# Performance work log

Measured on AMD Instinct MI355X. Metric: run time of the kernel, lower is better.

Reference implementation:

```python
import jax, jax.numpy as jnp
import numpy as np

N_NODES = 10000
N_EDGES = 160000
F_IN = 2613
D = 256
H = 4
NEG_SLOPE = 0.2
BN_EPS = 1e-5


def _bn(h, g, b):
    # BatchNorm1d in training mode: batch statistics, biased variance
    return (h - h.mean(0)) / jnp.sqrt(h.var(0) + BN_EPS) * g + b


def _gat_conv(h_in, src, dst, n, W, att_src, att_dst, bias):
    # PyG GATConv, concat=True: h_in [n, F] -> [n, H*D]
    h = (h_in @ W).reshape(n, H, D)                      # [n, H, D]
    a_src = jnp.sum(h * att_src, axis=-1)                # [n, H]
    a_dst = jnp.sum(h * att_dst, axis=-1)                # [n, H]
    e = jax.nn.leaky_relu(a_src[src] + a_dst[dst], NEG_SLOPE)  # [E, H]
    # segment softmax over destination nodes (stable)
    m = jax.ops.segment_max(e, dst, num_segments=n)
    e = jnp.exp(e - m[dst])
    denom = jax.ops.segment_sum(e, dst, num_segments=n)
    alpha = e / (denom[dst] + 1e-16)                     # [E, H]
    out = jax.ops.segment_sum(h[src] * alpha[:, :, None], dst, num_segments=n)
    return out.reshape(n, H * D) + bias


def setup_inputs() -> dict:
    key = jax.random.key(0)
    ks = jax.random.split(key, 24)
    s = 0.02
    inp = {
        "x": jax.random.normal(ks[0], (N_NODES, F_IN), jnp.float32),
        "edges": jax.random.randint(ks[1], (2, N_EDGES), 0, N_NODES, jnp.int64),
        # MLP stack
        "W1": jax.random.normal(ks[2], (F_IN, D), jnp.float32) * s,
        "b1": jnp.zeros((D,), jnp.float32),
        "W2": jax.random.normal(ks[3], (D, D), jnp.float32) * s,
        "b2": jnp.zeros((D,), jnp.float32),
        "W3": jax.random.normal(ks[4], (D, D), jnp.float32) * s,
        "b3": jnp.zeros((D,), jnp.float32),
        # BatchNorm affine params
        "g1": jnp.ones((D,), jnp.float32), "be1": jnp.zeros((D,), jnp.float32),
        "g2": jnp.ones((D,), jnp.float32), "be2": jnp.zeros((D,), jnp.float32),
        "g3": jnp.ones((D,), jnp.float32), "be3": jnp.zeros((D,), jnp.float32),
        "g4": jnp.ones((H * D,), jnp.float32), "be4": jnp.zeros((H * D,), jnp.float32),
        "Wg1": jax.random.normal(ks[5], (D, H * D), jnp.float32) * s,
        "as1": jax.random.normal(ks[6], (H, D), jnp.float32) * s,
        "ad1": jax.random.normal(ks[7], (H, D), jnp.float32) * s,
        "bg1": jnp.zeros((H * D,), jnp.float32),
        "Wg2": jax.random.normal(ks[8], (H * D, H * D), jnp.float32) * s,
        "as2": jax.random.normal(ks[9], (H, D), jnp.float32) * s,
        "ad2": jax.random.normal(ks[10], (H, D), jnp.float32) * s,
        "bg2": jnp.zeros((H * D,), jnp.float32),
    }
    return inp


def reference(x, edges, W1, b1, W2, b2, W3, b3,
              g1, be1, g2, be2, g3, be3, g4, be4,
              Wg1, as1, ad1, bg1, Wg2, as2, ad2, bg2):
    n = x.shape[0]
    src, dst = edges[0], edges[1]
    # PyG: remove existing self-loops then add one per node. We reroute
    # accidental self-loops deterministically, then append self-loops.
    dst = jnp.where(src == dst, (dst + 1) % n, dst)
    loops = jnp.arange(n, dtype=src.dtype)
    src = jnp.concatenate([src, loops])
    dst = jnp.concatenate([dst, loops])

    h = jax.nn.elu(_bn(x @ W1 + b1, g1, be1))
    h = jax.nn.elu(_bn(h @ W2 + b2, g2, be2))
    h = jax.nn.elu(_bn(h @ W3 + b3, g3, be3))
    h = _gat_conv(h, src, dst, n, Wg1, as1, ad1, bg1)
    h = jax.nn.elu(_bn(h, g4, be4))
    h = _gat_conv(h, src, dst, n, Wg2, as2, ad2, bg2)
    return h
```

## Files before the change

kernel.cpp:

```cpp
#include <hip/hip_runtime.h>
#include <hip/hip_bf16.h>

typedef __attribute__((ext_vector_type(8))) short short8v;
typedef __attribute__((ext_vector_type(4))) float f32x4;

__device__ inline float b2f(ushort u) {
  union { uint i; float f; } c;
  c.i = (uint)u << 16;
  return c.f;
}
__device__ inline ushort f2b(float f) {
  __hip_bfloat16 h = __float2bfloat16(f);
  return *(ushort*)&h;
}

typedef __attribute__((address_space(1))) const unsigned int guint;
typedef __attribute__((address_space(3))) unsigned int luint;
__device__ __forceinline__ void gload16(const void* g, void* l) {
  __builtin_amdgcn_global_load_lds((guint*)g, (luint*)l, 16, 0, 0);
}

template <bool BN, bool ALIGNED, bool SPLIT>
__global__ __launch_bounds__(256) void gemm_bn(
    const float* __restrict__ A, const __hip_bfloat16* __restrict__ Bh,
    const __hip_bfloat16* __restrict__ Bl, const float* __restrict__ sc,
    const float* __restrict__ sh, float* __restrict__ P, int M, int N, int K,
    int Kp, int nc, int nr, int nz) {
  __shared__ ushort Ash[128][40];
  __shared__ ushort Asl[SPLIT ? 128 : 1][40];
  __shared__ ushort Bs2[2][128][32];
  __shared__ ushort Bl2[SPLIT ? 2 : 1][128][32];
  const int nwg = gridDim.x;
  const int b = blockIdx.x;
  const int l = (b & 7) * (nwg >> 3) + (b >> 3);
  const int cb = l % nc;
  const int rr = (l / nc) % nr;
  const int z = l / (nc * nr);

  const int tid = threadIdx.x;
  const int lane = tid & 63;
  const int w = tid >> 6, wr = w >> 1, wc = w & 1;
  const int brow = rr * 128, bcol = cb * 128;
  const int l15 = lane & 15, koff = (lane >> 4) * 8;
  const int arow = tid >> 1, aseg = (tid & 1) * 16;
  const int srow = tid >> 2, sseg = (tid & 3) * 8;
  const int nK = (K + 31) >> 5;
  const int ks0 = (nK * z) / nz, ks1 = (nK * (z + 1)) / nz;

  f32x4 acc[4][4] = {};

  const int ar = brow + arow;
  const bool arv = ar < M;
  const float* Arow = A + (long)ar * K;
  const ushort* gBh0 = (const ushort*)Bh + (long)(bcol + srow) * Kp + sseg;
  const ushort* gBh1 = (const ushort*)Bh + (long)(bcol + 64 + srow) * Kp + sseg;
  const ushort* gBl0 = SPLIT ? (const ushort*)Bl + (long)(bcol + srow) * Kp + sseg : nullptr;
  const ushort* gBl1 = SPLIT ? (const ushort*)Bl + (long)(bcol + 64 + srow) * Kp + sseg : nullptr;
  const int lo0 = (w * 64) << 3;
  const int lo1 = (256 + w * 64) << 3;

  float av[16];
  auto loadAv = [&](int ks) {
    const int kb = (ks << 5) + aseg;
    if (arv) {
      if (ALIGNED) {
        const float4* ap = (const float4*)(Arow + kb);
#pragma unroll
        for (int q = 0; q < 4; ++q) {
          float4 f = ap[q];
          av[q * 4 + 0] = f.x;
          av[q * 4 + 1] = f.y;
          av[q * 4 + 2] = f.z;
          av[q * 4 + 3] = f.w;
        }
      } else {
        if (kb + 16 <= K) {
#pragma unroll
          for (int j = 0; j < 16; ++j) av[j] = Arow[kb + j];
        } else {
#pragma unroll
          for (int j = 0; j < 16; ++j) av[j] = (kb + j < K) ? Arow[kb + j] : 0.f;
        }
      }
    } else {
#pragma unroll
      for (int j = 0; j < 16; ++j) av[j] = 0.f;
    }
  };

  if (ks0 < ks1) {
    loadAv(ks0);
    const int k0 = ks0 << 5;
    gload16(gBh0 + k0, &Bs2[0][0][0] + lo0);
    gload16(gBh1 + k0, &Bs2[0][0][0] + lo1);
    if (SPLIT) {
      gload16(gBl0 + k0, &Bl2[0][0][0] + lo0);
      gload16(gBl1 + k0, &Bl2[0][0][0] + lo1);
    }
  }

  for (int ks = ks0; ks < ks1; ++ks) {
    const int cur = (ks - ks0) & 1;
    const int kbase = (ks << 5) + aseg;
    if (BN && arv) {
#pragma unroll
      for (int q = 0; q < 4; ++q) {
        float4 c4 = *(const float4*)(sc + kbase + q * 4);
        float4 h4 = *(const float4*)(sh + kbase + q * 4);
        float* a4 = &av[q * 4];
        a4[0] = fmaf(a4[0], c4.x, h4.x);
        a4[1] = fmaf(a4[1], c4.y, h4.y);
        a4[2] = fmaf(a4[2], c4.z, h4.z);
        a4[3] = fmaf(a4[3], c4.w, h4.w);
      }
#pragma unroll
      for (int j = 0; j < 16; ++j) {
        float v = av[j];
        av[j] = v > 0.f ? v : (__expf(v) - 1.f);
      }
    }
    short8v ah0, ah1, al0, al1;
    if (SPLIT) {
#pragma unroll
      for (int j = 0; j < 8; ++j) {
        {
          uint u = __float_as_uint(av[j]);
          ah0[j] = (short)(u >> 16);
          al0[j] = (short)f2b(av[j] - __uint_as_float(u & 0xFFFF0000u));
        }
        {
          uint u = __float_as_uint(av[j + 8]);
          ah1[j] = (short)(u >> 16);
          al1[j] = (short)f2b(av[j + 8] - __uint_as_float(u & 0xFFFF0000u));
        }
      }
    } else {
#pragma unroll
      for (int j = 0; j < 8; ++j) {
        ah0[j] = (short)f2b(av[j]);
        ah1[j] = (short)f2b(av[j + 8]);
      }
    }
    __syncthreads();
    *(short8v*)&Ash[arow][aseg] = ah0;
    *(short8v*)&Ash[arow][aseg + 8] = ah1;
    if (SPLIT) {
      *(short8v*)&Asl[arow][aseg] = al0;
      *(short8v*)&Asl[arow][aseg + 8] = al1;
    }
    __syncthreads();
    if (ks + 1 < ks1) {
      const int k0n = (ks + 1) << 5;
      const int nxt = cur ^ 1;
      gload16(gBh0 + k0n, &Bs2[nxt][0][0] + lo0);
      gload16(gBh1 + k0n, &Bs2[nxt][0][0] + lo1);
      if (SPLIT) {
        gload16(gBl0 + k0n, &Bl2[nxt][0][0] + lo0);
        gload16(gBl1 + k0n, &Bl2[nxt][0][0] + lo1);
      }
      loadAv(ks + 1);
    }
    short8v bfh[4], bfl[4];
#pragma unroll
    for (int nn = 0; nn < 4; ++nn) {
      bfh[nn] = *(const short8v*)&Bs2[cur][wc * 64 + nn * 16 + l15][koff];
      if (SPLIT) bfl[nn] = *(const short8v*)&Bl2[cur][wc * 64 + nn * 16 + l15][koff];
    }
#pragma unroll
    for (int m = 0; m < 4; ++m) {
      short8v afh = *(const short8v*)&Ash[wr * 64 + m * 16 + l15][koff];
      short8v afl;
      if (SPLIT) afl = *(const short8v*)&Asl[wr * 64 + m * 16 + l15][koff];
#pragma unroll
      for (int nn = 0; nn < 4; ++nn) {
        acc[m][nn] = __builtin_amdgcn_mfma_f32_16x16x32_bf16(afh, bfh[nn], acc[m][nn], 0, 0, 0);
        if (SPLIT) {
          acc[m][nn] = __builtin_amdgcn_mfma_f32_16x16x32_bf16(afh, bfl[nn], acc[m][nn], 0, 0, 0);
          acc[m][nn] = __builtin_amdgcn_mfma_f32_16x16x32_bf16(afl, bfh[nn], acc[m][nn], 0, 0, 0);
        }
      }
    }
  }

  float* outp = P + (long)z * M * N;
#pragma unroll
  for (int m = 0; m < 4; ++m) {
#pragma unroll
    for (int nn = 0; nn < 4; ++nn) {
      int col = bcol + wc * 64 + nn * 16 + l15;
#pragma unroll
      for (int r = 0; r < 4; ++r) {
        int row = brow + wr * 64 + m * 16 + (lane >> 4) * 4 + r;
        if (row < M) outp[(long)row * N + col] = acc[m][nn][r];
      }
    }
  }
}

__global__ __launch_bounds__(256) void gemm_bf16(
    const ushort* __restrict__ A, const __hip_bfloat16* __restrict__ B,
    ushort* __restrict__ C, int M, int N, int K, int nc, int nr) {
  __shared__ ushort A2[2][128][32];
  __shared__ ushort B2[2][128][32];
  const int nwg = gridDim.x;
  const int b = blockIdx.x;
  const int l = (b & 7) * (nwg >> 3) + (b >> 3);
  const int cb = l % nc;
  const int rr = l / nc;

  const int tid = threadIdx.x;
  const int lane = tid & 63;
  const int w = tid >> 6, wr = w >> 1, wc = w & 1;
  const int brow = rr * 128, bcol = cb * 128;
  const int l15 = lane & 15, koff = (lane >> 4) * 8;
  const int srow = tid >> 2, sseg = (tid & 3) * 8;
  const int nK = K >> 5;

  f32x4 acc[4][4] = {};

  const ushort* gA0 = A + (long)(brow + srow) * K + sseg;
  const ushort* gA1 = A + (long)(brow + 64 + srow) * K + sseg;
  const ushort* gB0 = (const ushort*)B + (long)(bcol + srow) * K + sseg;
  const ushort* gB1 = (const ushort*)B + (long)(bcol + 64 + srow) * K + sseg;
  const int lo0 = (w * 64) << 3;
  const int lo1 = (256 + w * 64) << 3;

  gload16(gA0, &A2[0][0][0] + lo0);
  gload16(gA1, &A2[0][0][0] + lo1);
  gload16(gB0, &B2[0][0][0] + lo0);
  gload16(gB1, &B2[0][0][0] + lo1);

  for (int ks = 0; ks < nK; ++ks) {
    const int cur = ks & 1;
    __syncthreads();
    if (ks + 1 < nK) {
      const int k0n = (ks + 1) << 5;
      const int nxt = cur ^ 1;
      gload16(gA0 + k0n, &A2[nxt][0][0] + lo0);
      gload16(gA1 + k0n, &A2[nxt][0][0] + lo1);
      gload16(gB0 + k0n, &B2[nxt][0][0] + lo0);
      gload16(gB1 + k0n, &B2[nxt][0][0] + lo1);
    }
    short8v bf[4];
#pragma unroll
    for (int nn = 0; nn < 4; ++nn)
      bf[nn] = *(const short8v*)&B2[cur][wc * 64 + nn * 16 + l15][koff];
#pragma unroll
    for (int m = 0; m < 4; ++m) {
      short8v af = *(const short8v*)&A2[cur][wr * 64 + m * 16 + l15][koff];
#pragma unroll
      for (int nn = 0; nn < 4; ++nn)
        acc[m][nn] = __builtin_amdgcn_mfma_f32_16x16x32_bf16(af, bf[nn], acc[m][nn], 0, 0, 0);
    }
  }

#pragma unroll
  for (int m = 0; m < 4; ++m) {
#pragma unroll
    for (int nn = 0; nn < 4; ++nn) {
      int col = bcol + wc * 64 + nn * 16 + l15;
#pragma unroll
      for (int r = 0; r < 4; ++r) {
        int row = brow + wr * 64 + m * 16 + (lane >> 4) * 4 + r;
        if (row < M) C[(long)row * N + col] = f2b(acc[m][nn][r]);
      }
    }
  }
}

__global__ __launch_bounds__(256) void bn_elu_b16(
    const float* __restrict__ h, const float* __restrict__ sc,
    const float* __restrict__ sh, ushort* __restrict__ o, long MN, int N) {
  long nq = MN >> 2;
  for (long q = blockIdx.x * 256LL + threadIdx.x; q < nq;
       q += (long)gridDim.x * 256LL) {
    long i = q << 2;
    int col = (int)(i % N);
    float4 v = *(const float4*)(h + i);
    float4 c = *(const float4*)(sc + col);
    float4 s = *(const float4*)(sh + col);
    float a0 = fmaf(v.x, c.x, s.x);
    float a1 = fmaf(v.y, c.y, s.y);
    float a2 = fmaf(v.z, c.z, s.z);
    float a3 = fmaf(v.w, c.w, s.w);
    a0 = a0 > 0.f ? a0 : (__expf(a0) - 1.f);
    a1 = a1 > 0.f ? a1 : (__expf(a1) - 1.f);
    a2 = a2 > 0.f ? a2 : (__expf(a2) - 1.f);
    a3 = a3 > 0.f ? a3 : (__expf(a3) - 1.f);
    ushort4 r;
    r.x = f2b(a0);
    r.y = f2b(a1);
    r.z = f2b(a2);
    r.w = f2b(a3);
    *(ushort4*)(o + i) = r;
  }
}

template <bool BIAS, bool STATS>
__global__ __launch_bounds__(256) void reduce_post(
    const float* __restrict__ P, const float* __restrict__ bias,
    float* __restrict__ C, float* __restrict__ osum, float* __restrict__ osq,
    long MN, int N, int Z) {
  const int col = (int)((blockIdx.x * 256 + threadIdx.x) % N);
  const float bv = BIAS ? bias[col] : 0.f;
  float ps = 0.f, pq = 0.f;
  for (long i = blockIdx.x * 256LL + threadIdx.x; i < MN;
       i += (long)gridDim.x * 256LL) {
    float s = bv;
    for (int zz = 0; zz < Z; ++zz) s += P[(long)zz * MN + i];
    C[i] = s;
    if (STATS) {
      ps += s;
      pq += s * s;
    }
  }
  if (STATS) {
    atomicAdd(&osum[col], ps);
    atomicAdd(&osq[col], pq);
  }
}

__global__ __launch_bounds__(256) void bn_coef(
    const float* __restrict__ ssum, const float* __restrict__ ssq,
    const float* __restrict__ g, const float* __restrict__ be,
    float* __restrict__ sc, float* __restrict__ sh, int N, float invM) {
  int c = blockIdx.x * 256 + threadIdx.x;
  if (c >= N) return;
  float mean = ssum[c] * invM;
  float var = ssq[c] * invM - mean * mean;
  float s = rsqrtf(var + 1e-5f) * g[c];
  sc[c] = s;
  sh[c] = be[c] - mean * s;
}

template <bool LO>
__global__ __launch_bounds__(256) void trans_split(
    const float* __restrict__ W, __hip_bfloat16* __restrict__ Oh,
    __hip_bfloat16* __restrict__ Ol, int K, int N, int Kp) {
  __shared__ float tile[64][65];
  const int k0 = blockIdx.x * 64, n0 = blockIdx.y * 64;
  const int tx = threadIdx.x & 63, ty = threadIdx.x >> 6;
#pragma unroll
  for (int j = 0; j < 16; ++j) {
    int r = ty * 16 + j;
    int k = k0 + r;
    tile[r][tx] = (k < K) ? W[(long)k * N + n0 + tx] : 0.f;
  }
  __syncthreads();
#pragma unroll
  for (int j = 0; j < 16; ++j) {
    int a = ty * 16 + j;
    float v = tile[tx][a];
    long o = (long)(n0 + a) * Kp + k0 + tx;
    if (LO) {
      uint u = __float_as_uint(v);
      ushort hu = (ushort)(u >> 16);
      Oh[o] = *(__hip_bfloat16*)&hu;
      ushort lu = f2b(v - __uint_as_float(u & 0xFFFF0000u));
      Ol[o] = *(__hip_bfloat16*)&lu;
    } else {
      ushort hu = f2b(v);
      Oh[o] = *(__hip_bfloat16*)&hu;
    }
  }
}

__global__ __launch_bounds__(256) void bn_stats(
    const float* __restrict__ h, int M, int N, float* __restrict__ sum,
    float* __restrict__ sumsq) {
  int col = blockIdx.y * 256 + threadIdx.x;
  float s = 0.f, sq = 0.f;
  for (int r = blockIdx.x; r < M; r += gridDim.x) {
    float v = h[(long)r * N + col];
    s += v;
    sq += v * v;
  }
  atomicAdd(&sum[col], s);
  atomicAdd(&sumsq[col], sq);
}

__global__ __launch_bounds__(256) void att_scores_bf16(
    const ushort* __restrict__ hgb, const float* __restrict__ att_s,
    const float* __restrict__ att_d, float* __restrict__ a_src,
    float* __restrict__ a_dst, int n) {
  int node = blockIdx.x;
  int h = threadIdx.x >> 6, lane = threadIdx.x & 63;
  int c = lane * 4;
  ushort4 hv = *(const ushort4*)(hgb + (long)node * 1024 + h * 256 + c);
  float4 as = *(const float4*)(att_s + h * 256 + c);
  float4 ad = *(const float4*)(att_d + h * 256 + c);
  float x0 = b2f(hv.x), x1 = b2f(hv.y), x2 = b2f(hv.z), x3 = b2f(hv.w);
  float ss = x0 * as.x + x1 * as.y + x2 * as.z + x3 * as.w;
  float sd = x0 * ad.x + x1 * ad.y + x2 * ad.z + x3 * ad.w;
#pragma unroll
  for (int off = 32; off; off >>= 1) {
    ss += __shfl_down(ss, off);
    sd += __shfl_down(sd, off);
  }
  if (lane == 0) {
    a_src[node * 4 + h] = ss;
    a_dst[node * 4 + h] = sd;
  }
}

__global__ __launch_bounds__(256) void deg_count(
    const int* __restrict__ srcA, const int* __restrict__ dstA,
    int* __restrict__ deg, int n, int E0, int E) {
  int e = blockIdx.x * blockDim.x + threadIdx.x;
  if (e >= E) return;
  int d;
  if (e < E0) {
    int s = srcA[e];
    d = dstA[e];
    if (s == d) d = (d + 1) % n;
  } else {
    d = e - E0;
  }
  atomicAdd(&deg[d], 1);
}

__global__ __launch_bounds__(256) void scan_rows(
    const int* __restrict__ deg, int* __restrict__ row_start, int n) {
  __shared__ int sums[256];
  int t = threadIdx.x;
  int chunk = (n + 255) / 256;
  int start = t * chunk, end = min(start + chunk, n);
  int s = 0;
  for (int i = start; i < end; ++i) s += deg[i];
  sums[t] = s;
  __syncthreads();
  for (int off = 1; off < 256; off <<= 1) {
    int v = (t >= off) ? sums[t - off] : 0;
    __syncthreads();
    sums[t] += v;
    __syncthreads();
  }
  int run = (t == 0) ? 0 : sums[t - 1];
  for (int i = start; i < end; ++i) {
    row_start[i] = run;
    run += deg[i];
  }
  if (t == 255) row_start[n] = run;
}

__global__ __launch_bounds__(256) void scatter_edges(
    const int* __restrict__ srcA, const int* __restrict__ dstA,
    int* __restrict__ cursor, int* __restrict__ csr_src, int n, int E0, int E) {
  int e = blockIdx.x * blockDim.x + threadIdx.x;
  if (e >= E) return;
  int s, d;
  if (e < E0) {
    s = srcA[e];
    d = dstA[e];
    if (s == d) d = (d + 1) % n;
  } else {
    s = d = e - E0;
  }
  int pos = atomicAdd(&cursor[d], 1);
  csr_src[pos] = s;
}

__global__ __launch_bounds__(256) void aggregate_fused(
    const ushort* __restrict__ hgb, const int* __restrict__ row_start,
    const int* __restrict__ csr_src, const float* __restrict__ a_src,
    const float* __restrict__ a_dst, const float* __restrict__ bias,
    float* __restrict__ out) {
  int d = blockIdx.x;
  int t = threadIdx.x;
  int hh = t >> 6;
  int off = hh * 256 + (t & 63) * 4;
  int p0 = row_start[d], p1 = row_start[d + 1];
  float adv = a_dst[d * 4 + hh];
  float den = 1e-16f;
  float4 acc = {0.f, 0.f, 0.f, 0.f};
  for (int p = p0; p < p1; ++p) {
    int s = csr_src[p];
    float v = a_src[s * 4 + hh] + adv;
    v = v > 0.f ? v : 0.2f * v;
    float ex = __expf(v);
    den += ex;
    ushort4 hv = *(const ushort4*)(hgb + (long)s * 1024 + off);
    acc.x += ex * b2f(hv.x);
    acc.y += ex * b2f(hv.y);
    acc.z += ex * b2f(hv.z);
    acc.w += ex * b2f(hv.w);
  }
  float rden = 1.f / den;
  float4 bv = *(const float4*)(bias + off);
  float4 o;
  o.x = bv.x + acc.x * rden;
  o.y = bv.y + acc.y * rden;
  o.z = bv.z + acc.z * rden;
  o.w = bv.w + acc.w * rden;
  *(float4*)(out + (long)d * 1024 + off) = o;
}

extern "C" void kernel_launch(void* const* d_in, const int* in_sizes, int n_in,
                              void* d_out, int out_size, void* d_ws,
                              size_t ws_size, hipStream_t stream) {
  const float* x = (const float*)d_in[0];
  const int* edges = (const int*)d_in[1];
  const float* W1 = (const float*)d_in[2];
  const float* b1 = (const float*)d_in[3];
  const float* W2 = (const float*)d_in[4];
  const float* b2 = (const float*)d_in[5];
  const float* W3 = (const float*)d_in[6];
  const float* b3 = (const float*)d_in[7];
  const float* g1 = (const float*)d_in[8];
  const float* be1 = (const float*)d_in[9];
  const float* g2 = (const float*)d_in[10];
  const float* be2 = (const float*)d_in[11];
  const float* g3 = (const float*)d_in[12];
  const float* be3 = (const float*)d_in[13];
  const float* g4 = (const float*)d_in[14];
  const float* be4 = (const float*)d_in[15];
  const float* Wg1 = (const float*)d_in[16];
  const float* as1 = (const float*)d_in[17];
  const float* ad1 = (const float*)d_in[18];
  const float* bg1 = (const float*)d_in[19];
  const float* Wg2 = (const float*)d_in[20];
  const float* as2 = (const float*)d_in[21];
  const float* ad2 = (const float*)d_in[22];
  const float* bg2 = (const float*)d_in[23];
  float* out = (float*)d_out;

  const int n = 10000, E0 = 160000, E = 170000;
  const int F = 2613, Fp = 2624, D = 256, HD = 1024;
  const int* srcA = edges;
  const int* dstA = edges + E0;

  uint8_t* p = (uint8_t*)d_ws;
  auto alloc = [&](size_t bytes) -> void* {
    void* r = (void*)p;
    p += (bytes + 255) & ~(size_t)255;
    return r;
  };
  float* h1 = (float*)alloc((size_t)n * D * 4);
  float* h2 = (float*)alloc((size_t)n * D * 4);
  float* h3 = (float*)alloc((size_t)n * D * 4);
  float* agg = (float*)alloc((size_t)n * HD * 4);
  float* pbuf = (float*)alloc((size_t)4 * n * D * 4);
  ushort* hgb = (ushort*)alloc((size_t)n * HD * 2);
  ushort* actb = (ushort*)alloc((size_t)n * HD * 2);
  __hip_bfloat16* W1h = (__hip_bfloat16*)alloc((size_t)D * Fp * 2);
  __hip_bfloat16* W2h = (__hip_bfloat16*)alloc((size_t)D * D * 2);
  __hip_bfloat16* W2l = (__hip_bfloat16*)alloc((size_t)D * D * 2);
  __hip_bfloat16* W3h = (__hip_bfloat16*)alloc((size_t)D * D * 2);
  __hip_bfloat16* W3l = (__hip_bfloat16*)alloc((size_t)D * D * 2);
  __hip_bfloat16* Wg1h = (__hip_bfloat16*)alloc((size_t)HD * D * 2);
  __hip_bfloat16* Wg2h = (__hip_bfloat16*)alloc((size_t)HD * HD * 2);
  float* asrc = (float*)alloc((size_t)n * 4 * 4);
  float* adst = (float*)alloc((size_t)n * 4 * 4);
  float* sc1 = (float*)alloc(D * 4);
  float* sh1 = (float*)alloc(D * 4);
  float* sc2 = (float*)alloc(D * 4);
  float* sh2 = (float*)alloc(D * 4);
  float* sc3 = (float*)alloc(D * 4);
  float* sh3 = (float*)alloc(D * 4);
  float* sc4 = (float*)alloc(HD * 4);
  float* sh4 = (float*)alloc(HD * 4);
  int* row_start = (int*)alloc((size_t)(n + 1) * 4);
  int* cursor = (int*)alloc((size_t)n * 4);
  int* csr_src = (int*)alloc((size_t)E * 4);
  uint8_t* z0 = p;
  float* ssum1 = (float*)alloc(D * 4);
  float* ssq1 = (float*)alloc(D * 4);
  float* ssum2 = (float*)alloc(D * 4);
  float* ssq2 = (float*)alloc(D * 4);
  float* ssum3 = (float*)alloc(D * 4);
  float* ssq3 = (float*)alloc(D * 4);
  float* ssum4 = (float*)alloc(HD * 4);
  float* ssq4 = (float*)alloc(HD * 4);
  int* deg = (int*)alloc((size_t)n * 4);
  size_t zbytes = (size_t)(p - z0);

  dim3 blk(256);
  const int rb = (n + 127) / 128;
  const int eb = (E + 255) / 256;
  const long MN_D = (long)n * D;
  const long MN_HD = (long)n * HD;
  const float invM = 1.f / (float)n;
  const int gMLP = 2 * rb * 4;
  const int gGAT = 8 * rb;

  hipMemsetAsync(z0, 0, zbytes, stream);

  deg_count<<<eb, blk, 0, stream>>>(srcA, dstA, deg, n, E0, E);
  scan_rows<<<1, blk, 0, stream>>>(deg, row_start, n);
  hipMemcpyAsync(cursor, row_start, n * sizeof(int), hipMemcpyDeviceToDevice, stream);
  scatter_edges<<<eb, blk, 0, stream>>>(srcA, dstA, cursor, csr_src, n, E0, E);

  trans_split<false><<<dim3(Fp / 64, D / 64), blk, 0, stream>>>(W1, W1h, nullptr, F, D, Fp);
  trans_split<true><<<dim3(D / 64, D / 64), blk, 0, stream>>>(W2, W2h, W2l, D, D, D);
  trans_split<true><<<dim3(D / 64, D / 64), blk, 0, stream>>>(W3, W3h, W3l, D, D, D);
  trans_split<false><<<dim3(D / 64, HD / 64), blk, 0, stream>>>(Wg1, Wg1h, nullptr, D, HD, D);
  trans_split<false><<<dim3(HD / 64, HD / 64), blk, 0, stream>>>(Wg2, Wg2h, nullptr, HD, HD, HD);

  gemm_bn<false, false, false><<<gMLP, blk, 0, stream>>>(
      x, W1h, nullptr, nullptr, nullptr, pbuf, n, D, F, Fp, 2, rb, 4);
  reduce_post<true, true><<<512, blk, 0, stream>>>(pbuf, b1, h1, ssum1, ssq1, MN_D, D, 4);
  bn_coef<<<1, blk, 0, stream>>>(ssum1, ssq1, g1, be1, sc1, sh1, D, invM);

  gemm_bn<true, true, true><<<gMLP, blk, 0, stream>>>(
      h1, W2h, W2l, sc1, sh1, pbuf, n, D, D, D, 2, rb, 4);
  reduce_post<true, true><<<512, blk, 0, stream>>>(pbuf, b2, h2, ssum2, ssq2, MN_D, D, 4);
  bn_coef<<<1, blk, 0, stream>>>(ssum2, ssq2, g2, be2, sc2, sh2, D, invM);

  gemm_bn<true, true, true><<<gMLP, blk, 0, stream>>>(
      h2, W3h, W3l, sc2, sh2, pbuf, n, D, D, D, 2, rb, 4);
  reduce_post<true, true><<<512, blk, 0, stream>>>(pbuf, b3, h3, ssum3, ssq3, MN_D, D, 4);
  bn_coef<<<1, blk, 0, stream>>>(ssum3, ssq3, g3, be3, sc3, sh3, D, invM);

  bn_elu_b16<<<1024, blk, 0, stream>>>(h3, sc3, sh3, actb, MN_D, D);
  gemm_bf16<<<gGAT, blk, 0, stream>>>(actb, Wg1h, hgb, n, HD, D, 8, rb);
  att_scores_bf16<<<n, blk, 0, stream>>>(hgb, as1, ad1, asrc, adst, n);
  aggregate_fused<<<n, blk, 0, stream>>>(hgb, row_start, csr_src, asrc, adst, bg1, agg);

  bn_stats<<<dim3(64, HD / 256), blk, 0, stream>>>(agg, n, HD, ssum4, ssq4);
  bn_coef<<<4, blk, 0, stream>>>(ssum4, ssq4, g4, be4, sc4, sh4, HD, invM);
  bn_elu_b16<<<2048, blk, 0, stream>>>(agg, sc4, sh4, actb, MN_HD, HD);

  gemm_bf16<<<gGAT, blk, 0, stream>>>(actb, Wg2h, hgb, n, HD, HD, 8, rb);
  att_scores_bf16<<<n, blk, 0, stream>>>(hgb, as2, ad2, asrc, adst, n);
  aggregate_fused<<<n, blk, 0, stream>>>(hgb, row_start, csr_src, asrc, adst, bg2, out);
}
```

Baseline: 534.7 us.

## Drop split-bf16 weights for MLP layers 2-3 and raise layer-1 split-K to 8

Removes the hi/lo bf16 split for W2 and W3, so those GEMMs use a single bf16 weight and skip the extra low-part MFMA pass. The layer-1 GEMM over the long K dimension now splits K eight ways instead of four, with a larger partial buffer and the reduction summing eight partials. This adds parallelism to the dominant GEMM at the cost of more partial-sum traffic, and it lowers accuracy for layers 2-3.

After: 554.7 us. 1.04x slower.

```diff
diff --git a/kernel.cpp b/kernel.cpp
--- a/kernel.cpp
+++ b/kernel.cpp
@@ -333,10 +333,9 @@
   sh[c] = be[c] - mean * s;
 }
 
-template <bool LO>
-__global__ __launch_bounds__(256) void trans_split(
-    const float* __restrict__ W, __hip_bfloat16* __restrict__ Oh,
-    __hip_bfloat16* __restrict__ Ol, int K, int N, int Kp) {
+__global__ __launch_bounds__(256) void trans_b16(
+    const float* __restrict__ W, __hip_bfloat16* __restrict__ Oh, int K, int N,
+    int Kp) {
   __shared__ float tile[64][65];
   const int k0 = blockIdx.x * 64, n0 = blockIdx.y * 64;
   const int tx = threadIdx.x & 63, ty = threadIdx.x >> 6;
@@ -351,17 +350,8 @@
   for (int j = 0; j < 16; ++j) {
     int a = ty * 16 + j;
     float v = tile[tx][a];
-    long o = (long)(n0 + a) * Kp + k0 + tx;
-    if (LO) {
-      uint u = __float_as_uint(v);
-      ushort hu = (ushort)(u >> 16);
-      Oh[o] = *(__hip_bfloat16*)&hu;
-      ushort lu = f2b(v - __uint_as_float(u & 0xFFFF0000u));
-      Ol[o] = *(__hip_bfloat16*)&lu;
-    } else {
-      ushort hu = f2b(v);
-      Oh[o] = *(__hip_bfloat16*)&hu;
-    }
+    ushort hu = f2b(v);
+    Oh[(long)(n0 + a) * Kp + k0 + tx] = *(__hip_bfloat16*)&hu;
   }
 }
 
@@ -539,14 +529,12 @@
   float* h2 = (float*)alloc((size_t)n * D * 4);
   float* h3 = (float*)alloc((size_t)n * D * 4);
   float* agg = (float*)alloc((size_t)n * HD * 4);
-  float* pbuf = (float*)alloc((size_t)4 * n * D * 4);
+  float* pbuf = (float*)alloc((size_t)8 * n * D * 4);
   ushort* hgb = (ushort*)alloc((size_t)n * HD * 2);
   ushort* actb = (ushort*)alloc((size_t)n * HD * 2);
   __hip_bfloat16* W1h = (__hip_bfloat16*)alloc((size_t)D * Fp * 2);
   __hip_bfloat16* W2h = (__hip_bfloat16*)alloc((size_t)D * D * 2);
-  __hip_bfloat16* W2l = (__hip_bfloat16*)alloc((size_t)D * D * 2);
   __hip_bfloat16* W3h = (__hip_bfloat16*)alloc((size_t)D * D * 2);
-  __hip_bfloat16* W3l = (__hip_bfloat16*)alloc((size_t)D * D * 2);
   __hip_bfloat16* Wg1h = (__hip_bfloat16*)alloc((size_t)HD * D * 2);
   __hip_bfloat16* Wg2h = (__hip_bfloat16*)alloc((size_t)HD * HD * 2);
   float* asrc = (float*)alloc((size_t)n * 4 * 4);
@@ -580,6 +568,7 @@
   const long MN_D = (long)n * D;
   const long MN_HD = (long)n * HD;
   const float invM = 1.f / (float)n;
+  const int gL1 = 2 * rb * 8;
   const int gMLP = 2 * rb * 4;
   const int gGAT = 8 * rb;
 
@@ -590,24 +579,24 @@
   hipMemcpyAsync(cursor, row_start, n * sizeof(int), hipMemcpyDeviceToDevice, stream);
   scatter_edges<<<eb, blk, 0, stream>>>(srcA, dstA, cursor, csr_src, n, E0, E);
 
-  trans_split<false><<<dim3(Fp / 64, D / 64), blk, 0, stream>>>(W1, W1h, nullptr, F, D, Fp);
-  trans_split<true><<<dim3(D / 64, D / 64), blk, 0, stream>>>(W2, W2h, W2l, D, D, D);
-  trans_split<true><<<dim3(D / 64, D / 64), blk, 0, stream>>>(W3, W3h, W3l, D, D, D);
-  trans_split<false><<<dim3(D / 64, HD / 64), blk, 0, stream>>>(Wg1, Wg1h, nullptr, D, HD, D);
-  trans_split<false><<<dim3(HD / 64, HD / 64), blk, 0, stream>>>(Wg2, Wg2h, nullptr, HD, HD, HD);
-
-  gemm_bn<false, false, false><<<gMLP, blk, 0, stream>>>(
-      x, W1h, nullptr, nullptr, nullptr, pbuf, n, D, F, Fp, 2, rb, 4);
-  reduce_post<true, true><<<512, blk, 0, stream>>>(pbuf, b1, h1, ssum1, ssq1, MN_D, D, 4);
+  trans_b16<<<dim3(Fp / 64, D / 64), blk, 0, stream>>>(W1, W1h, F, D, Fp);
+  trans_b16<<<dim3(D / 64, D / 64), blk, 0, stream>>>(W2, W2h, D, D, D);
+  trans_b16<<<dim3(D / 64, D / 64), blk, 0, stream>>>(W3, W3h, D, D, D);
+  trans_b16<<<dim3(D / 64, HD / 64), blk, 0, stream>>>(Wg1, Wg1h, D, HD, D);
+  trans_b16<<<dim3(HD / 64, HD / 64), blk, 0, stream>>>(Wg2, Wg2h, HD, HD, HD);
+
+  gemm_bn<false, false, false><<<gL1, blk, 0, stream>>>(
+      x, W1h, nullptr, nullptr, nullptr, pbuf, n, D, F, Fp, 2, rb, 8);
+  reduce_post<true, true><<<512, blk, 0, stream>>>(pbuf, b1, h1, ssum1, ssq1, MN_D, D, 8);
   bn_coef<<<1, blk, 0, stream>>>(ssum1, ssq1, g1, be1, sc1, sh1, D, invM);
 
-  gemm_bn<true, true, true><<<gMLP, blk, 0, stream>>>(
-      h1, W2h, W2l, sc1, sh1, pbuf, n, D, D, D, 2, rb, 4);
+  gemm_bn<true, true, false><<<gMLP, blk, 0, stream>>>(
+      h1, W2h, nullptr, sc1, sh1, pbuf, n, D, D, D, 2, rb, 4);
   reduce_post<true, true><<<512, blk, 0, stream>>>(pbuf, b2, h2, ssum2, ssq2, MN_D, D, 4);
   bn_coef<<<1, blk, 0, stream>>>(ssum2, ssq2, g2, be2, sc2, sh2, D, invM);
 
-  gemm_bn<true, true, true><<<gMLP, blk, 0, stream>>>(
-      h2, W3h, W3l, sc2, sh2, pbuf, n, D, D, D, 2, rb, 4);
+  gemm_bn<true, true, false><<<gMLP, blk, 0, stream>>>(
+      h2, W3h, nullptr, sc2, sh2, pbuf, n, D, D, D, 2, rb, 4);
   reduce_post<true, true><<<512, blk, 0, stream>>>(pbuf, b3, h3, ssum3, ssq3, MN_D, D, 4);
   bn_coef<<<1, blk, 0, stream>>>(ssum3, ssq3, g3, be3, sc3, sh3, D, invM);
 
```
